# Performance work log

Measured on AMD Instinct MI355X. Metric: run time of the kernel, lower is better.

Reference implementation:

```python
import jax, jax.numpy as jnp
import numpy as np

EPS = 1e-5

def _bn(h, g, b, m, v):
    # inference-mode batchnorm, channel axis = 1
    shape = (1, -1) + (1,) * (h.ndim - 2)
    scale = g.reshape(shape) / jnp.sqrt(v.reshape(shape) + EPS)
    return (h - m.reshape(shape)) * scale + b.reshape(shape)

def setup_inputs() -> dict:
    B, Cin, Cout, N, K = 2, 64, 64, 50000, 16
    key = jax.random.key(0)
    ks = jax.random.split(key, 24)
    def bn_params(i, C):
        g = 1.0 + 0.1 * jax.random.normal(ks[i], (C,), jnp.float32)
        b = 0.1 * jax.random.normal(ks[i + 1], (C,), jnp.float32)
        m = 0.1 * jax.random.normal(ks[i + 2], (C,), jnp.float32)
        v = jax.random.uniform(ks[i + 3], (C,), jnp.float32, 0.5, 1.5)
        return g, b, m, v
    bn0_g, bn0_b, bn0_m, bn0_v = bn_params(0, Cin)
    bn2a_g, bn2a_b, bn2a_m, bn2a_v = bn_params(4, Cin)
    bn2b_g, bn2b_b, bn2b_m, bn2b_v = bn_params(8, Cout)
    x = jax.random.normal(ks[12], (B, Cin, N), jnp.float32)
    neighbors = jax.random.randint(ks[13], (B, K, N), 0, N, jnp.int32)
    w1 = 0.05 * jax.random.normal(ks[14], (Cout, Cin), jnp.float32)
    b1 = 0.05 * jax.random.normal(ks[15], (Cout,), jnp.float32)
    w2a = 0.05 * jax.random.normal(ks[16], (Cout, Cin), jnp.float32)
    w2b = 0.05 * jax.random.normal(ks[17], (Cout, Cout), jnp.float32)
    wf = 0.05 * jax.random.normal(ks[18], (Cout, 2 * Cout), jnp.float32)
    bf = 0.05 * jax.random.normal(ks[19], (Cout,), jnp.float32)
    return {"x": x, "neighbors": neighbors,
            "bn0_g": bn0_g, "bn0_b": bn0_b, "bn0_m": bn0_m, "bn0_v": bn0_v,
            "w1": w1, "b1": b1,
            "bn2a_g": bn2a_g, "bn2a_b": bn2a_b, "bn2a_m": bn2a_m, "bn2a_v": bn2a_v,
            "w2a": w2a,
            "bn2b_g": bn2b_g, "bn2b_b": bn2b_b, "bn2b_m": bn2b_m, "bn2b_v": bn2b_v,
            "w2b": w2b, "wf": wf, "bf": bf}

def reference(x, neighbors, bn0_g, bn0_b, bn0_m, bn0_v, w1, b1,
              bn2a_g, bn2a_b, bn2a_m, bn2a_v, w2a,
              bn2b_g, bn2b_b, bn2b_m, bn2b_v, w2b, wf, bf):
    # x: (B, Cin, N), neighbors: (B, K, N) int indices into N
    xn = _bn(x, bn0_g, bn0_b, bn0_m, bn0_v)                    # BatchNorm1d
    point = jnp.einsum('oc,bcn->bon', w1, xn) + b1[None, :, None]  # conv1 (1x1)
    idx = neighbors[:, 1:, :]                                   # (B, K-1, N); skip self (col 0)
    # gathered[b,c,k,n] = xn[b,c, idx[b,k,n]]
    gathered = jax.vmap(lambda xb, ib: xb[:, ib])(xn, idx)      # (B, C, K-1, N)
    diff = jnp.transpose(gathered, (0, 1, 3, 2)) - xn[:, :, :, None]  # (B, C, N, K-1)
    h = _bn(diff, bn2a_g, bn2a_b, bn2a_m, bn2a_v)               # BatchNorm2d
    h = jnp.einsum('oc,bcnk->bonk', w2a, h)                     # Conv2d 1x1, no bias
    h = jax.nn.relu(_bn(h, bn2b_g, bn2b_b, bn2b_m, bn2b_v))
    h = jnp.einsum('oc,bcnk->bonk', w2b, h)                     # Conv2d 1x1, no bias
    neigh = h.max(axis=-1)                                      # max over K-1 neighbors
    cat = jnp.concatenate([point, neigh], axis=1)               # (B, 2*Cout, N)
    return jnp.einsum('oc,bcn->bon', wf, cat) + bf[None, :, None]
```

## Files before the change

kernel.cpp:

```cpp
#include <hip/hip_runtime.h>
#include <hip/hip_bf16.h>

typedef __bf16 bf16x8 __attribute__((ext_vector_type(8)));
typedef float f32x4 __attribute__((ext_vector_type(4)));
typedef unsigned int uint32x4 __attribute__((ext_vector_type(4)));

#define NPT 50000

#define OFF_Y    0u
#define OFF_PRM  12800000u
#define OFF_W2   12801024u
#define OFF_WP   12809216u
#define OFF_W2B  12817408u
#define OFF_WN   12825600u
#define OFF_FLAG 12833792u

__device__ __forceinline__ int detect_bf16(const void* bn0_v) {
    const unsigned short* u = (const unsigned short*)bn0_v;
    int cnt = 0;
    for (int i = 0; i < 64; ++i) {
        float f = __uint_as_float(((unsigned int)u[i]) << 16);
        if (f > 0.4f && f < 1.6f) cnt++;
    }
    return (cnt >= 60) ? 1 : 0;
}

__global__ __launch_bounds__(256) void precompute_kernel(
    const void* bn0_g, const void* bn0_b, const void* bn0_m, const void* bn0_v,
    const void* w1, const void* b1,
    const void* bn2a_g, const void* bn2a_b, const void* bn2a_m, const void* bn2a_v,
    const void* w2a,
    const void* bn2b_g, const void* bn2b_b, const void* bn2b_m, const void* bn2b_v,
    const void* w2b, const void* wf, const void* bfv,
    float* __restrict__ prm, __bf16* __restrict__ W2bf, __bf16* __restrict__ Wpbf,
    __bf16* __restrict__ W2Bbf, __bf16* __restrict__ Wnbf, int* __restrict__ flagp)
{
    __shared__ int sflag;
    int t = threadIdx.x;
    if (t == 0) sflag = detect_bf16(bn0_v);
    __syncthreads();
    int fl = sflag;

    if (blockIdx.x < 16) {
        __shared__ __bf16 w1s[4096];
        __shared__ float wfr[4][64];
        int ob = blockIdx.x * 4;
        if (fl) {
            const __bf16* W1 = (const __bf16*)w1;
            const __bf16* WF = (const __bf16*)wf;
            for (int i = t; i < 4096; i += 256) w1s[i] = W1[i];
            if (t < 256) {
                int o = t >> 6, m = t & 63;
                wfr[o][m] = (float)WF[(ob + o) * 128 + m];
            }
        } else {
            const float* W1 = (const float*)w1;
            const float* WF = (const float*)wf;
            for (int i = t; i < 4096; i += 256) w1s[i] = (__bf16)W1[i];
            if (t < 256) {
                int o = t >> 6, m = t & 63;
                wfr[o][m] = WF[(ob + o) * 128 + m];
            }
        }
        __syncthreads();
        int o = t >> 6, c = t & 63;
        float acc = 0.f;
        for (int m = 0; m < 64; ++m)
            acc += wfr[o][m] * (float)w1s[m * 64 + c];
        Wpbf[(ob + o) * 64 + c] = (__bf16)acc;
        return;
    }

    __shared__ __bf16 wfs[8192];
    __shared__ __bf16 w2as[4096];
    __shared__ float b1s[64], bfs[64], s2a[64], t2a[64], s2b[64], t2b[64];

    if (t == 0) *flagp = fl;

    if (fl) {
        const __bf16* W2A = (const __bf16*)w2a;
        const __bf16* WF  = (const __bf16*)wf;
        const __bf16* W2B = (const __bf16*)w2b;
        for (int i = t; i < 4096; i += 256) { w2as[i] = W2A[i]; W2Bbf[i] = W2B[i]; }
        for (int i = t; i < 8192; i += 256) wfs[i] = WF[i];
        if (t < 64) {
            float s0 = (float)((const __bf16*)bn0_g)[t] / sqrtf((float)((const __bf16*)bn0_v)[t] + 1e-5f);
            prm[t] = s0;
            prm[64 + t] = (float)((const __bf16*)bn0_b)[t] - (float)((const __bf16*)bn0_m)[t] * s0;
            float sa = (float)((const __bf16*)bn2a_g)[t] / sqrtf((float)((const __bf16*)bn2a_v)[t] + 1e-5f);
            s2a[t] = sa;
            t2a[t] = (float)((const __bf16*)bn2a_b)[t] - (float)((const __bf16*)bn2a_m)[t] * sa;
            float sb = (float)((const __bf16*)bn2b_g)[t] / sqrtf((float)((const __bf16*)bn2b_v)[t] + 1e-5f);
            s2b[t] = sb;
            t2b[t] = (float)((const __bf16*)bn2b_b)[t] - (float)((const __bf16*)bn2b_m)[t] * sb;
            b1s[t] = (float)((const __bf16*)b1)[t];
            bfs[t] = (float)((const __bf16*)bfv)[t];
        }
    } else {
        const float* W2A = (const float*)w2a;
        const float* WF  = (const float*)wf;
        const float* W2B = (const float*)w2b;
        for (int i = t; i < 4096; i += 256) { w2as[i] = (__bf16)W2A[i]; W2Bbf[i] = (__bf16)W2B[i]; }
        for (int i = t; i < 8192; i += 256) wfs[i] = (__bf16)WF[i];
        if (t < 64) {
            float s0 = ((const float*)bn0_g)[t] / sqrtf(((const float*)bn0_v)[t] + 1e-5f);
            prm[t] = s0;
            prm[64 + t] = ((const float*)bn0_b)[t] - ((const float*)bn0_m)[t] * s0;
            float sa = ((const float*)bn2a_g)[t] / sqrtf(((const float*)bn2a_v)[t] + 1e-5f);
            s2a[t] = sa;
            t2a[t] = ((const float*)bn2a_b)[t] - ((const float*)bn2a_m)[t] * sa;
            float sb = ((const float*)bn2b_g)[t] / sqrtf(((const float*)bn2b_v)[t] + 1e-5f);
            s2b[t] = sb;
            t2b[t] = ((const float*)bn2b_b)[t] - ((const float*)bn2b_m)[t] * sb;
            b1s[t] = ((const float*)b1)[t];
            bfs[t] = ((const float*)bfv)[t];
        }
    }
    __syncthreads();

    for (int e = t; e < 4096; e += 256) {
        int o = e >> 6, c = e & 63;
        W2bf[e] = (__bf16)((float)w2as[e] * s2a[c] * s2b[o]);
        Wnbf[e] = wfs[o * 128 + 64 + c];
    }
    if (t < 64) {
        float acc = 0.f, accb = 0.f;
        for (int c = 0; c < 64; ++c) {
            acc  += (float)w2as[t * 64 + c] * t2a[c];
            accb += (float)wfs[t * 128 + c] * b1s[c];
        }
        prm[128 + t] = s2b[t] * acc + t2b[t];
        prm[192 + t] = accb + bfs[t];
    }
}

__global__ __launch_bounds__(256) void pass1_kernel(
    const void* x, const float* __restrict__ prm,
    const __bf16* __restrict__ W2bf, __bf16* __restrict__ Y,
    const int* __restrict__ flagp)
{
    __shared__ float xs[64][65];
    int bid = blockIdx.x;
    int b = bid / 782;
    int n0 = (bid % 782) * 64;
    int npts = NPT - n0; if (npts > 64) npts = 64;
    int fl = *flagp;

    if (npts == 64) {
        if (fl) {
            const __bf16* xb = (const __bf16*)x + (size_t)b * 64 * NPT + n0;
            for (int i = threadIdx.x; i < 512; i += 256) {
                int c = i >> 3, q = (i & 7) * 8;
                bf16x8 v = *(const bf16x8*)(xb + (size_t)c * NPT + q);
                #pragma unroll
                for (int e = 0; e < 8; ++e)
                    xs[q + e][c] = fmaf((float)v[e], prm[c], prm[64 + c]);
            }
        } else {
            const float* xb = (const float*)x + (size_t)b * 64 * NPT + n0;
            for (int i = threadIdx.x; i < 1024; i += 256) {
                int c = i >> 4, q = (i & 15) * 4;
                float4 v = *(const float4*)(xb + (size_t)c * NPT + q);
                xs[q + 0][c] = fmaf(v.x, prm[c], prm[64 + c]);
                xs[q + 1][c] = fmaf(v.y, prm[c], prm[64 + c]);
                xs[q + 2][c] = fmaf(v.z, prm[c], prm[64 + c]);
                xs[q + 3][c] = fmaf(v.w, prm[c], prm[64 + c]);
            }
        }
    } else {
        if (fl) {
            const __bf16* xb = (const __bf16*)x + (size_t)b * 64 * NPT;
            for (int i = threadIdx.x; i < 4096; i += 256) {
                int c = i >> 6, p = i & 63;
                float v = (p < npts) ? (float)xb[(size_t)c * NPT + n0 + p] : 0.f;
                xs[p][c] = fmaf(v, prm[c], prm[64 + c]);
            }
        } else {
            const float* xb = (const float*)x + (size_t)b * 64 * NPT;
            for (int i = threadIdx.x; i < 4096; i += 256) {
                int c = i >> 6, p = i & 63;
                float v = (p < npts) ? xb[(size_t)c * NPT + n0 + p] : 0.f;
                xs[p][c] = fmaf(v, prm[c], prm[64 + c]);
            }
        }
    }
    __syncthreads();

    int wid = threadIdx.x >> 6, lane = threadIdx.x & 63;
    int pl = (wid << 4) + (lane & 15);
    int hq = lane >> 4;
    int c0 = hq << 3;

    bf16x8 a0, a1;
    #pragma unroll
    for (int i = 0; i < 8; ++i) {
        a0[i] = (__bf16)xs[pl][c0 + i];
        a1[i] = (__bf16)xs[pl][c0 + 32 + i];
    }

    int ob = lane & 15;
    f32x4 accY[4];
    #pragma unroll
    for (int nt = 0; nt < 4; ++nt) {
        bf16x8 w20 = *(const bf16x8*)(W2bf + (ob + 16 * nt) * 64 + c0);
        bf16x8 w21 = *(const bf16x8*)(W2bf + (ob + 16 * nt) * 64 + c0 + 32);
        f32x4 z = {0.f, 0.f, 0.f, 0.f};
        accY[nt] = __builtin_amdgcn_mfma_f32_16x16x32_bf16(a0, w20, z, 0, 0, 0);
        accY[nt] = __builtin_amdgcn_mfma_f32_16x16x32_bf16(a1, w21, accY[nt], 0, 0, 0);
    }

    #pragma unroll
    for (int nt = 0; nt < 4; ++nt) {
        #pragma unroll
        for (int i = 0; i < 4; ++i) {
            int prow = (wid << 4) + (hq << 2) + i;
            if (prow < npts)
                Y[((size_t)b * NPT + n0 + prow) * 64 + ob + 16 * nt] = (__bf16)accY[nt][i];
        }
    }
}

__global__ __launch_bounds__(256, 4) void pass2_kernel(
    const int* __restrict__ nbr, const __bf16* __restrict__ Y,
    const void* x, const float* __restrict__ prm,
    const __bf16* __restrict__ W2Bbf, const __bf16* __restrict__ Wnbf,
    const __bf16* __restrict__ Wpbf, void* out, const int* __restrict__ flagp)
{
    __shared__ float ns[4][16][69];
    int h = threadIdx.x >> 6, lane = threadIdx.x & 63;
    int gtile = blockIdx.x;
    int b = gtile / 3125;
    int n0 = (gtile % 3125) << 4;
    int fl = *flagp;

    int mo = lane & 15;
    int hq = lane >> 4;
    int c0 = hq << 3;
    int nglob = n0 + mo;

    const int* nb_base = nbr + (size_t)b * 16 * NPT + nglob;
    unsigned int ju[4];
    #pragma unroll
    for (int kk = 0; kk < 4; ++kk) {
        int kv = 4 * h + kk + 1; if (kv > 15) kv = 15;
        unsigned long long a = (unsigned long long)(nb_base + (size_t)kv * NPT);
        asm volatile("global_load_dword %0, %1, off" : "=v"(ju[kk]) : "v"(a) : "memory");
    }

    const __bf16* yrow = Y + ((size_t)b * NPT + nglob) * 64;
    bf16x8 yn0 = *(const bf16x8*)(yrow + c0);
    bf16x8 yn1 = *(const bf16x8*)(yrow + c0 + 32);
    bf16x8 wA[4][2];
    #pragma unroll
    for (int mt = 0; mt < 4; ++mt) {
        wA[mt][0] = *(const bf16x8*)(W2Bbf + (mo + 16 * mt) * 64 + c0);
        wA[mt][1] = *(const bf16x8*)(W2Bbf + (mo + 16 * mt) * 64 + c0 + 32);
    }

    asm volatile("s_waitcnt vmcnt(0)" ::: "memory");
    __builtin_amdgcn_sched_barrier(0);

    uint32x4 g0[4], g1[4];
    const char* ybase = (const char*)Y + (size_t)b * NPT * 128 + hq * 16;
    #pragma unroll
    for (int kk = 0; kk < 4; ++kk) {
        unsigned long long a0 = (unsigned long long)(ybase + (size_t)ju[kk] * 128);
        asm volatile("global_load_dwordx4 %0, %1, off" : "=v"(g0[kk]) : "v"(a0) : "memory");
        asm volatile("global_load_dwordx4 %0, %1, off offset:64" : "=v"(g1[kk]) : "v"(a0) : "memory");
    }

    float mv0[8], mv1[8];
    #pragma unroll
    for (int i = 0; i < 8; ++i) {
        mv0[i] = prm[128 + c0 + i]      - (float)yn0[i];
        mv1[i] = prm[128 + c0 + 32 + i] - (float)yn1[i];
    }

    f32x4 vmax[4];
    #pragma unroll
    for (int mt = 0; mt < 4; ++mt) vmax[mt] = {-3.0e38f, -3.0e38f, -3.0e38f, -3.0e38f};

    asm volatile("s_waitcnt vmcnt(0)" ::: "memory");
    __builtin_amdgcn_sched_barrier(0);

    #pragma unroll
    for (int kk = 0; kk < 4; ++kk) {
        bf16x8 y0 = __builtin_bit_cast(bf16x8, g0[kk]);
        bf16x8 y1 = __builtin_bit_cast(bf16x8, g1[kk]);
        bf16x8 t0, t1;
        #pragma unroll
        for (int i = 0; i < 8; ++i) {
            t0[i] = (__bf16)fmaxf((float)y0[i] + mv0[i], 0.f);
            t1[i] = (__bf16)fmaxf((float)y1[i] + mv1[i], 0.f);
        }
        #pragma unroll
        for (int mt = 0; mt < 4; ++mt) {
            f32x4 hh = {0.f, 0.f, 0.f, 0.f};
            hh = __builtin_amdgcn_mfma_f32_16x16x32_bf16(wA[mt][0], t0, hh, 0, 0, 0);
            hh = __builtin_amdgcn_mfma_f32_16x16x32_bf16(wA[mt][1], t1, hh, 0, 0, 0);
            #pragma unroll
            for (int i = 0; i < 4; ++i) vmax[mt][i] = fmaxf(vmax[mt][i], hh[i]);
        }
    }

    #pragma unroll
    for (int mt = 0; mt < 4; ++mt)
        #pragma unroll
        for (int i = 0; i < 4; ++i)
            ns[h][mo][16 * mt + (hq << 2) + i] = vmax[mt][i];

    __syncthreads();

    if (h < 2) {
        bf16x8 nb2[2];
        #pragma unroll
        for (int ks = 0; ks < 2; ++ks)
            #pragma unroll
            for (int i = 0; i < 8; ++i) {
                int c = c0 + 32 * ks + i;
                float m01 = fmaxf(ns[0][mo][c], ns[1][mo][c]);
                float m23 = fmaxf(ns[2][mo][c], ns[3][mo][c]);
                nb2[ks][i] = (__bf16)fmaxf(m01, m23);
            }

        bf16x8 xnb[2];
        if (fl) {
            const __bf16* xp = (const __bf16*)x + (size_t)b * 64 * NPT + nglob;
            #pragma unroll
            for (int ks = 0; ks < 2; ++ks)
                #pragma unroll
                for (int i = 0; i < 8; ++i) {
                    int c = c0 + 32 * ks + i;
                    float v = (float)xp[(size_t)c * NPT];
                    xnb[ks][i] = (__bf16)fmaf(v, prm[c], prm[64 + c]);
                }
        } else {
            const float* xp = (const float*)x + (size_t)b * 64 * NPT + nglob;
            #pragma unroll
            for (int ks = 0; ks < 2; ++ks)
                #pragma unroll
                for (int i = 0; i < 8; ++i) {
                    int c = c0 + 32 * ks + i;
                    float v = xp[(size_t)c * NPT];
                    xnb[ks][i] = (__bf16)fmaf(v, prm[c], prm[64 + c]);
                }
        }

        #pragma unroll
        for (int q = 0; q < 2; ++q) {
            int mt = 2 * h + q;
            bf16x8 wn0 = *(const bf16x8*)(Wnbf + (mo + 16 * mt) * 64 + c0);
            bf16x8 wn1 = *(const bf16x8*)(Wnbf + (mo + 16 * mt) * 64 + c0 + 32);
            bf16x8 wp0 = *(const bf16x8*)(Wpbf + (mo + 16 * mt) * 64 + c0);
            bf16x8 wp1 = *(const bf16x8*)(Wpbf + (mo + 16 * mt) * 64 + c0 + 32);
            f32x4 acc = *(const f32x4*)(prm + 192 + 16 * mt + 4 * hq);
            acc = __builtin_amdgcn_mfma_f32_16x16x32_bf16(wp0, xnb[0], acc, 0, 0, 0);
            acc = __builtin_amdgcn_mfma_f32_16x16x32_bf16(wp1, xnb[1], acc, 0, 0, 0);
            acc = __builtin_amdgcn_mfma_f32_16x16x32_bf16(wn0, nb2[0], acc, 0, 0, 0);
            acc = __builtin_amdgcn_mfma_f32_16x16x32_bf16(wn1, nb2[1], acc, 0, 0, 0);

            if (fl) {
                __bf16* ob = (__bf16*)out + (size_t)b * 64 * NPT + nglob;
                #pragma unroll
                for (int i = 0; i < 4; ++i)
                    ob[(size_t)(16 * mt + (hq << 2) + i) * NPT] = (__bf16)acc[i];
            } else {
                float* ob = (float*)out + (size_t)b * 64 * NPT + nglob;
                #pragma unroll
                for (int i = 0; i < 4; ++i)
                    ob[(size_t)(16 * mt + (hq << 2) + i) * NPT] = acc[i];
            }
        }
    }
}

extern "C" void kernel_launch(void* const* d_in, const int* in_sizes, int n_in,
                              void* d_out, int out_size, void* d_ws, size_t ws_size,
                              hipStream_t stream) {
    const void* x      = d_in[0];
    const int*  nbr    = (const int*)d_in[1];

    char* ws = (char*)d_ws;
    __bf16* Y     = (__bf16*)(ws + OFF_Y);
    float*  prm   = (float*)(ws + OFF_PRM);
    __bf16* W2bf  = (__bf16*)(ws + OFF_W2);
    __bf16* Wpbf  = (__bf16*)(ws + OFF_WP);
    __bf16* W2Bbf = (__bf16*)(ws + OFF_W2B);
    __bf16* Wnbf  = (__bf16*)(ws + OFF_WN);
    int*    flagp = (int*)(ws + OFF_FLAG);

    precompute_kernel<<<17, 256, 0, stream>>>(
        d_in[2], d_in[3], d_in[4], d_in[5], d_in[6], d_in[7],
        d_in[8], d_in[9], d_in[10], d_in[11], d_in[12],
        d_in[13], d_in[14], d_in[15], d_in[16], d_in[17], d_in[18], d_in[19],
        prm, W2bf, Wpbf, W2Bbf, Wnbf, flagp);

    pass1_kernel<<<1564, 256, 0, stream>>>(x, prm, W2bf, Y, flagp);

    pass2_kernel<<<6250, 256, 0, stream>>>(nbr, Y, x, prm, W2Bbf, Wnbf, Wpbf, d_out, flagp);
}
```

Baseline: 211.9 us.

## Store gathered intermediate Y in FP8 and restructure pass2 into two-tile blocks

The intermediate Y table is now stored as FP8 e4m3 with an interleaved channel layout instead of bf16. This halves the bytes per random neighbor gather, so each lane fetches one 16-byte load per neighbor. Pass2 blocks now process two 16-point tiles, with each wave pair covering 7-8 neighbors, and all four waves do the final projection. Block indices are remapped to interleave the two batches (XCD-style swizzle). The FP8 quantization of Y adds numerical error that may exceed tolerance, and one neighbor is processed redundantly by both halves.

```diff
diff --git a/kernel.cpp b/kernel.cpp
--- a/kernel.cpp
+++ b/kernel.cpp
@@ -1,5 +1,6 @@
 #include <hip/hip_runtime.h>
 #include <hip/hip_bf16.h>
+#include <hip/hip_fp8.h>
 
 typedef __bf16 bf16x8 __attribute__((ext_vector_type(8)));
 typedef float f32x4 __attribute__((ext_vector_type(4)));
@@ -7,13 +8,13 @@
 
 #define NPT 50000
 
-#define OFF_Y    0u
-#define OFF_PRM  12800000u
-#define OFF_W2   12801024u
-#define OFF_WP   12809216u
-#define OFF_W2B  12817408u
-#define OFF_WN   12825600u
-#define OFF_FLAG 12833792u
+#define OFF_Y8   0u
+#define OFF_PRM  6400000u
+#define OFF_W2   6401024u
+#define OFF_WP   6409216u
+#define OFF_W2B  6417408u
+#define OFF_WN   6425600u
+#define OFF_FLAG 6433792u
 
 __device__ __forceinline__ int detect_bf16(const void* bn0_v) {
     const unsigned short* u = (const unsigned short*)bn0_v;
@@ -23,6 +24,20 @@
         if (f > 0.4f && f < 1.6f) cnt++;
     }
     return (cnt >= 60) ? 1 : 0;
+}
+
+__device__ __forceinline__ unsigned char fp8_enc(float f) {
+    __hip_fp8_e4m3 v(f);
+    return (unsigned char)v.__x;
+}
+__device__ __forceinline__ float fp8_dec(unsigned char u) {
+    __hip_fp8_e4m3 v;
+    v.__x = (__hip_fp8_storage_t)u;
+    return (float)v;
+}
+__device__ __forceinline__ int ch_pos(int ch) {
+    return (ch < 32) ? (16 * (ch >> 3) + (ch & 7))
+                     : (16 * ((ch - 32) >> 3) + 8 + ((ch - 32) & 7));
 }
 
 __global__ __launch_bounds__(256) void precompute_kernel(
@@ -49,18 +64,14 @@
             const __bf16* W1 = (const __bf16*)w1;
             const __bf16* WF = (const __bf16*)wf;
             for (int i = t; i < 4096; i += 256) w1s[i] = W1[i];
-            if (t < 256) {
-                int o = t >> 6, m = t & 63;
-                wfr[o][m] = (float)WF[(ob + o) * 128 + m];
-            }
+            int o = t >> 6, m = t & 63;
+            wfr[o][m] = (float)WF[(ob + o) * 128 + m];
         } else {
             const float* W1 = (const float*)w1;
             const float* WF = (const float*)wf;
             for (int i = t; i < 4096; i += 256) w1s[i] = (__bf16)W1[i];
-            if (t < 256) {
-                int o = t >> 6, m = t & 63;
-                wfr[o][m] = WF[(ob + o) * 128 + m];
-            }
+            int o = t >> 6, m = t & 63;
+            wfr[o][m] = WF[(ob + o) * 128 + m];
         }
         __syncthreads();
         int o = t >> 6, c = t & 63;
@@ -136,13 +147,15 @@
 
 __global__ __launch_bounds__(256) void pass1_kernel(
     const void* x, const float* __restrict__ prm,
-    const __bf16* __restrict__ W2bf, __bf16* __restrict__ Y,
+    const __bf16* __restrict__ W2bf, unsigned char* __restrict__ Y8,
     const int* __restrict__ flagp)
 {
     __shared__ float xs[64][65];
-    int bid = blockIdx.x;
-    int b = bid / 782;
-    int n0 = (bid % 782) * 64;
+    int r = blockIdx.x & 7, g = blockIdx.x >> 3;
+    int b = r >> 2;
+    int blk = g * 4 + (r & 3);
+    if (blk >= 782) return;
+    int n0 = blk * 64;
     int npts = NPT - n0; if (npts > 64) npts = 64;
     int fl = *flagp;
 
@@ -211,45 +224,49 @@
 
     #pragma unroll
     for (int nt = 0; nt < 4; ++nt) {
+        int pos = ch_pos(ob + 16 * nt);
         #pragma unroll
         for (int i = 0; i < 4; ++i) {
             int prow = (wid << 4) + (hq << 2) + i;
             if (prow < npts)
-                Y[((size_t)b * NPT + n0 + prow) * 64 + ob + 16 * nt] = (__bf16)accY[nt][i];
-        }
-    }
-}
-
-__global__ __launch_bounds__(256, 4) void pass2_kernel(
-    const int* __restrict__ nbr, const __bf16* __restrict__ Y,
+                Y8[((size_t)b * NPT + n0 + prow) * 64 + pos] = fp8_enc(accY[nt][i]);
+        }
+    }
+}
+
+__global__ __launch_bounds__(256, 2) void pass2_kernel(
+    const int* __restrict__ nbr, const unsigned char* __restrict__ Y8,
     const void* x, const float* __restrict__ prm,
     const __bf16* __restrict__ W2Bbf, const __bf16* __restrict__ Wnbf,
     const __bf16* __restrict__ Wpbf, void* out, const int* __restrict__ flagp)
 {
-    __shared__ float ns[4][16][69];
-    int h = threadIdx.x >> 6, lane = threadIdx.x & 63;
-    int gtile = blockIdx.x;
-    int b = gtile / 3125;
-    int n0 = (gtile % 3125) << 4;
+    __shared__ float ns[2][2][16][69];
+    int wid = threadIdx.x >> 6, lane = threadIdx.x & 63;
+    int tile = wid >> 1, h = wid & 1;
+    int r = blockIdx.x & 7, g = blockIdx.x >> 3;
+    int b = r >> 2;
+    int tpair = g * 4 + (r & 3);
+    if (tpair >= 1563) return;
+    int n0 = tpair * 32 + (tile << 4);
     int fl = *flagp;
 
     int mo = lane & 15;
     int hq = lane >> 4;
     int c0 = hq << 3;
     int nglob = n0 + mo;
-
-    const int* nb_base = nbr + (size_t)b * 16 * NPT + nglob;
-    unsigned int ju[4];
-    #pragma unroll
-    for (int kk = 0; kk < 4; ++kk) {
-        int kv = 4 * h + kk + 1; if (kv > 15) kv = 15;
-        unsigned long long a = (unsigned long long)(nb_base + (size_t)kv * NPT);
+    int ng = (nglob < NPT) ? nglob : (NPT - 1);
+
+    const int* nb_base = nbr + (size_t)b * 16 * NPT + ng;
+    int kbase = h * 7;
+    unsigned int ju[8];
+    #pragma unroll
+    for (int kk = 0; kk < 8; ++kk) {
+        unsigned long long a = (unsigned long long)(nb_base + (size_t)(kbase + kk + 1) * NPT);
         asm volatile("global_load_dword %0, %1, off" : "=v"(ju[kk]) : "v"(a) : "memory");
     }
 
-    const __bf16* yrow = Y + ((size_t)b * NPT + nglob) * 64;
-    bf16x8 yn0 = *(const bf16x8*)(yrow + c0);
-    bf16x8 yn1 = *(const bf16x8*)(yrow + c0 + 32);
+    const unsigned char* yrow = Y8 + ((size_t)b * NPT + ng) * 64 + hq * 16;
+    uint32x4 own = *(const uint32x4*)yrow;
     bf16x8 wA[4][2];
     #pragma unroll
     for (int mt = 0; mt < 4; ++mt) {
@@ -260,20 +277,22 @@
     asm volatile("s_waitcnt vmcnt(0)" ::: "memory");
     __builtin_amdgcn_sched_barrier(0);
 
-    uint32x4 g0[4], g1[4];
-    const char* ybase = (const char*)Y + (size_t)b * NPT * 128 + hq * 16;
-    #pragma unroll
-    for (int kk = 0; kk < 4; ++kk) {
-        unsigned long long a0 = (unsigned long long)(ybase + (size_t)ju[kk] * 128);
-        asm volatile("global_load_dwordx4 %0, %1, off" : "=v"(g0[kk]) : "v"(a0) : "memory");
-        asm volatile("global_load_dwordx4 %0, %1, off offset:64" : "=v"(g1[kk]) : "v"(a0) : "memory");
+    uint32x4 gv[8];
+    const unsigned char* ybase = Y8 + (size_t)b * NPT * 64 + hq * 16;
+    #pragma unroll
+    for (int kk = 0; kk < 8; ++kk) {
+        unsigned long long a0 = (unsigned long long)(ybase + (size_t)ju[kk] * 64);
+        asm volatile("global_load_dwordx4 %0, %1, off" : "=v"(gv[kk]) : "v"(a0) : "memory");
     }
 
     float mv0[8], mv1[8];
     #pragma unroll
-    for (int i = 0; i < 8; ++i) {
-        mv0[i] = prm[128 + c0 + i]      - (float)yn0[i];
-        mv1[i] = prm[128 + c0 + 32 + i] - (float)yn1[i];
+    for (int s = 0; s < 8; ++s) {
+        unsigned u0 = (own[s >> 2] >> (8 * (s & 3))) & 0xFF;
+        int t1i = 8 + s;
+        unsigned u1 = (own[t1i >> 2] >> (8 * (t1i & 3))) & 0xFF;
+        mv0[s] = prm[128 + c0 + s]      - fp8_dec((unsigned char)u0);
+        mv1[s] = prm[128 + 32 + c0 + s] - fp8_dec((unsigned char)u1);
     }
 
     f32x4 vmax[4];
@@ -284,14 +303,15 @@
     __builtin_amdgcn_sched_barrier(0);
 
     #pragma unroll
-    for (int kk = 0; kk < 4; ++kk) {
-        bf16x8 y0 = __builtin_bit_cast(bf16x8, g0[kk]);
-        bf16x8 y1 = __builtin_bit_cast(bf16x8, g1[kk]);
+    for (int kk = 0; kk < 8; ++kk) {
         bf16x8 t0, t1;
         #pragma unroll
-        for (int i = 0; i < 8; ++i) {
-            t0[i] = (__bf16)fmaxf((float)y0[i] + mv0[i], 0.f);
-            t1[i] = (__bf16)fmaxf((float)y1[i] + mv1[i], 0.f);
+        for (int s = 0; s < 8; ++s) {
+            unsigned u0 = (gv[kk][s >> 2] >> (8 * (s & 3))) & 0xFF;
+            int t1i = 8 + s;
+            unsigned u1 = (gv[kk][t1i >> 2] >> (8 * (t1i & 3))) & 0xFF;
+            t0[s] = (__bf16)fmaxf(fp8_dec((unsigned char)u0) + mv0[s], 0.f);
+            t1[s] = (__bf16)fmaxf(fp8_dec((unsigned char)u1) + mv1[s], 0.f);
         }
         #pragma unroll
         for (int mt = 0; mt < 4; ++mt) {
@@ -307,58 +327,56 @@
     for (int mt = 0; mt < 4; ++mt)
         #pragma unroll
         for (int i = 0; i < 4; ++i)
-            ns[h][mo][16 * mt + (hq << 2) + i] = vmax[mt][i];
+            ns[tile][h][mo][16 * mt + (hq << 2) + i] = vmax[mt][i];
 
     __syncthreads();
 
-    if (h < 2) {
-        bf16x8 nb2[2];
+    bf16x8 nb2[2];
+    #pragma unroll
+    for (int ks = 0; ks < 2; ++ks)
+        #pragma unroll
+        for (int i = 0; i < 8; ++i) {
+            int c = c0 + 32 * ks + i;
+            nb2[ks][i] = (__bf16)fmaxf(ns[tile][0][mo][c], ns[tile][1][mo][c]);
+        }
+
+    bf16x8 xnb[2];
+    if (fl) {
+        const __bf16* xp = (const __bf16*)x + (size_t)b * 64 * NPT + ng;
         #pragma unroll
         for (int ks = 0; ks < 2; ++ks)
             #pragma unroll
             for (int i = 0; i < 8; ++i) {
                 int c = c0 + 32 * ks + i;
-                float m01 = fmaxf(ns[0][mo][c], ns[1][mo][c]);
-                float m23 = fmaxf(ns[2][mo][c], ns[3][mo][c]);
-                nb2[ks][i] = (__bf16)fmaxf(m01, m23);
-            }
-
-        bf16x8 xnb[2];
-        if (fl) {
-            const __bf16* xp = (const __bf16*)x + (size_t)b * 64 * NPT + nglob;
+                float v = (float)xp[(size_t)c * NPT];
+                xnb[ks][i] = (__bf16)fmaf(v, prm[c], prm[64 + c]);
+            }
+    } else {
+        const float* xp = (const float*)x + (size_t)b * 64 * NPT + ng;
+        #pragma unroll
+        for (int ks = 0; ks < 2; ++ks)
             #pragma unroll
-            for (int ks = 0; ks < 2; ++ks)
-                #pragma unroll
-                for (int i = 0; i < 8; ++i) {
-                    int c = c0 + 32 * ks + i;
-                    float v = (float)xp[(size_t)c * NPT];
-                    xnb[ks][i] = (__bf16)fmaf(v, prm[c], prm[64 + c]);
-                }
-        } else {
-            const float* xp = (const float*)x + (size_t)b * 64 * NPT + nglob;
-            #pragma unroll
-            for (int ks = 0; ks < 2; ++ks)
-                #pragma unroll
-                for (int i = 0; i < 8; ++i) {
-                    int c = c0 + 32 * ks + i;
-                    float v = xp[(size_t)c * NPT];
-                    xnb[ks][i] = (__bf16)fmaf(v, prm[c], prm[64 + c]);
-                }
-        }
-
-        #pragma unroll
-        for (int q = 0; q < 2; ++q) {
-            int mt = 2 * h + q;
-            bf16x8 wn0 = *(const bf16x8*)(Wnbf + (mo + 16 * mt) * 64 + c0);
-            bf16x8 wn1 = *(const bf16x8*)(Wnbf + (mo + 16 * mt) * 64 + c0 + 32);
-            bf16x8 wp0 = *(const bf16x8*)(Wpbf + (mo + 16 * mt) * 64 + c0);
-            bf16x8 wp1 = *(const bf16x8*)(Wpbf + (mo + 16 * mt) * 64 + c0 + 32);
-            f32x4 acc = *(const f32x4*)(prm + 192 + 16 * mt + 4 * hq);
-            acc = __builtin_amdgcn_mfma_f32_16x16x32_bf16(wp0, xnb[0], acc, 0, 0, 0);
-            acc = __builtin_amdgcn_mfma_f32_16x16x32_bf16(wp1, xnb[1], acc, 0, 0, 0);
-            acc = __builtin_amdgcn_mfma_f32_16x16x32_bf16(wn0, nb2[0], acc, 0, 0, 0);
-            acc = __builtin_amdgcn_mfma_f32_16x16x32_bf16(wn1, nb2[1], acc, 0, 0, 0);
-
+            for (int i = 0; i < 8; ++i) {
+                int c = c0 + 32 * ks + i;
+                float v = xp[(size_t)c * NPT];
+                xnb[ks][i] = (__bf16)fmaf(v, prm[c], prm[64 + c]);
+            }
+    }
+
+    #pragma unroll
+    for (int q = 0; q < 2; ++q) {
+        int mt = 2 * h + q;
+        bf16x8 wn0 = *(const bf16x8*)(Wnbf + (mo + 16 * mt) * 64 + c0);
+        bf16x8 wn1 = *(const bf16x8*)(Wnbf + (mo + 16 * mt) * 64 + c0 + 32);
+        bf16x8 wp0 = *(const bf16x8*)(Wpbf + (mo + 16 * mt) * 64 + c0);
+        bf16x8 wp1 = *(const bf16x8*)(Wpbf + (mo + 16 * mt) * 64 + c0 + 32);
+        f32x4 acc = *(const f32x4*)(prm + 192 + 16 * mt + 4 * hq);
+        acc = __builtin_amdgcn_mfma_f32_16x16x32_bf16(wp0, xnb[0], acc, 0, 0, 0);
+        acc = __builtin_amdgcn_mfma_f32_16x16x32_bf16(wp1, xnb[1], acc, 0, 0, 0);
+        acc = __builtin_amdgcn_mfma_f32_16x16x32_bf16(wn0, nb2[0], acc, 0, 0, 0);
+        acc = __builtin_amdgcn_mfma_f32_16x16x32_bf16(wn1, nb2[1], acc, 0, 0, 0);
+
+        if (nglob < NPT) {
             if (fl) {
                 __bf16* ob = (__bf16*)out + (size_t)b * 64 * NPT + nglob;
                 #pragma unroll
@@ -381,7 +399,7 @@
     const int*  nbr    = (const int*)d_in[1];
 
     char* ws = (char*)d_ws;
-    __bf16* Y     = (__bf16*)(ws + OFF_Y);
+    unsigned char* Y8 = (unsigned char*)(ws + OFF_Y8);
     float*  prm   = (float*)(ws + OFF_PRM);
     __bf16* W2bf  = (__bf16*)(ws + OFF_W2);
     __bf16* Wpbf  = (__bf16*)(ws + OFF_WP);
@@ -395,7 +413,7 @@
         d_in[13], d_in[14], d_in[15], d_in[16], d_in[17], d_in[18], d_in[19],
         prm, W2bf, Wpbf, W2Bbf, Wnbf, flagp);
 
-    pass1_kernel<<<1564, 256, 0, stream>>>(x, prm, W2bf, Y, flagp);
-
-    pass2_kernel<<<6250, 256, 0, stream>>>(nbr, Y, x, prm, W2Bbf, Wnbf, Wpbf, d_out, flagp);
-}
+    pass1_kernel<<<1568, 256, 0, stream>>>(x, prm, W2bf, Y8, flagp);
+
+    pass2_kernel<<<3128, 256, 0, stream>>>(nbr, Y8, x, prm, W2Bbf, Wnbf, Wpbf, d_out, flagp);
+}
```

Result: faster. 176.4 us (-16.8%).
